# Kernel optimization log

Measured on AMD Instinct MI355X. Metric: run time of the kernel, lower is better.

## Reference

```python
import jax, jax.numpy as jnp
import numpy as np

SIGMA = 0.1
B, C, H, W = 2, 3, 64, 64


def setup_inputs() -> dict:
    key = jax.random.key(0)
    x = jax.random.uniform(key, (B, C, H, W), dtype=jnp.float32)
    return {"x": x}


def reference(x) -> jnp.ndarray:
    """Range-only bilateral filter: out[p] = sum_q K(p,q) x[q] / sum_q K(p,q),
    K(p,q) = exp(-((x_q - x_p)/sigma)^2), all-pairs over the H*W pixels,
    independently per (batch, channel)."""
    b, c, h, w = x.shape
    n = h * w
    xf = x.reshape(b, c, n)                      # [B,C,N]
    # pairwise intensity differences -> Gaussian range kernel [B,C,N,N]
    diff = xf[:, :, :, None] - xf[:, :, None, :]
    K = jnp.exp(-jnp.square(diff / SIGMA))
    num = jnp.einsum('bcpq,bcq->bcp', K, xf)     # weighted sum over source pixels
    den = jnp.sum(K, axis=-1)                    # normalization
    return (num / den).reshape(b, c, h, w)
```

## Files before the change

kernel.cpp:

```cpp
#include <hip/hip_runtime.h>

#define NSLICE 6
#define NPIX   4096
#define M      20

#define C0         0.088622693f
#define TWO_C0     0.177245385f
#define AEXP_LOG2  0.035597112f
#define DEN0       362.99854f

__global__ __launch_bounds__(256) void moments_kernel(
        const float* __restrict__ x, float* __restrict__ ws) {
    const int mi = blockIdx.x;
    const int s  = blockIdx.y;
    const float fm = (float)(mi + 1);
    const int tid = threadIdx.x;
    const float4* x4 = (const float4*)(x + s * NPIX);

    float Sc = 0.f, Ss = 0.f, Tc = 0.f, Ts = 0.f, X = 0.f;
    #pragma unroll
    for (int j = 0; j < NPIX / 4 / 256; ++j) {
        float4 v4 = x4[j * 256 + tid];
        float vv[4] = {v4.x, v4.y, v4.z, v4.w};
        #pragma unroll
        for (int k = 0; k < 4; ++k) {
            float v   = vv[k];
            float arg = 0.5f * fm * v;
            float sn  = __builtin_amdgcn_sinf(arg);
            float cn  = __builtin_amdgcn_cosf(arg);
            Sc += cn;  Ss += sn;
            Tc = fmaf(v, cn, Tc);
            Ts = fmaf(v, sn, Ts);
            X += v;
        }
    }

    #pragma unroll
    for (int off = 1; off < 64; off <<= 1) {
        Sc += __shfl_xor(Sc, off);  Ss += __shfl_xor(Ss, off);
        Tc += __shfl_xor(Tc, off);  Ts += __shfl_xor(Ts, off);
        X  += __shfl_xor(X,  off);
    }
    __shared__ float red[4][5];
    const int w = tid >> 6;
    if ((tid & 63) == 0) {
        red[w][0] = Sc; red[w][1] = Ss; red[w][2] = Tc; red[w][3] = Ts; red[w][4] = X;
    }
    __syncthreads();
    if (tid == 0) {
        float sc = 0.f, ss = 0.f, tc = 0.f, ts = 0.f, xx = 0.f;
        #pragma unroll
        for (int ww = 0; ww < 4; ++ww) {
            sc += red[ww][0]; ss += red[ww][1]; tc += red[ww][2];
            ts += red[ww][3]; xx += red[ww][4];
        }
        float coef = TWO_C0 * __builtin_amdgcn_exp2f(-AEXP_LOG2 * fm * fm);
        float* f = ws + (s * (M + 1) + (mi + 1)) * 4;
        f[0] = coef * sc;  f[1] = coef * ss;
        f[2] = coef * tc;  f[3] = coef * ts;
        if (mi == 0) {
            float* f0 = ws + s * (M + 1) * 4;
            f0[0] = DEN0;  f0[1] = C0 * xx;  f0[2] = 0.f;  f0[3] = 0.f;
        }
    }
}

__global__ __launch_bounds__(512) void recombine_kernel(
        const float* __restrict__ x, const float* __restrict__ ws,
        float* __restrict__ out) {
    const int s = blockIdx.y;
    const int p = blockIdx.x * 512 + threadIdx.x;
    __shared__ __align__(16) float fin[(M + 1) * 4];
    if (threadIdx.x < (M + 1) * 4)
        fin[threadIdx.x] = ws[s * (M + 1) * 4 + threadIdx.x];
    __syncthreads();

    const float v  = x[s * NPIX + p];
    const float s1 = __builtin_amdgcn_sinf(0.5f * v);
    const float c1 = __builtin_amdgcn_cosf(0.5f * v);
    const float4* F = (const float4*)fin;

    float4 f0 = F[0], f1 = F[1];
    float den = f0.x, num = f0.y;
    den = fmaf(c1, f1.x, den);  den = fmaf(s1, f1.y, den);
    num = fmaf(c1, f1.z, num);  num = fmaf(s1, f1.w, num);

    const float tc = c1 + c1;
    float cm2 = 1.f, sm2 = 0.f, cm1 = c1, sm1 = s1;
    #pragma unroll
    for (int m = 2; m <= M; ++m) {
        float cn = fmaf(tc, cm1, -cm2);
        float sn = fmaf(tc, sm1, -sm2);
        cm2 = cm1; cm1 = cn; sm2 = sm1; sm1 = sn;
        float4 f = F[m];
        den = fmaf(cn, f.x, den);  den = fmaf(sn, f.y, den);
        num = fmaf(cn, f.z, num);  num = fmaf(sn, f.w, num);
    }
    out[s * NPIX + p] = num / den;
}

extern "C" void kernel_launch(void* const* d_in, const int* in_sizes, int n_in,
                              void* d_out, int out_size, void* d_ws, size_t ws_size,
                              hipStream_t stream) {
    const float* x = (const float*)d_in[0];
    float* out = (float*)d_out;
    float* ws  = (float*)d_ws;
    moments_kernel<<<dim3(M, NSLICE), dim3(256), 0, stream>>>(x, ws);
    recombine_kernel<<<dim3(NPIX / 512, NSLICE), dim3(512), 0, stream>>>(x, ws, out);
}
```

Before: 54.59 us.

## Fuse moments and recombine kernels into one launch with redundant per-block moments

Merges the two kernels into a single launch with 48 blocks. Each block recomputes all 20 Fourier moments for its slice before evaluating its 512 output pixels, so no workspace round-trip and no second launch are needed. Within the moment pass each thread covers 5 harmonics using a Chebyshev recurrence seeded from a few sin/cos calls, instead of one harmonic per block. The cost is that every block redoes the full moment reduction over 4096 pixels, which is eight times redundant work per slice.

```diff
diff --git a/kernel.cpp b/kernel.cpp
--- a/kernel.cpp
+++ b/kernel.cpp
@@ -3,90 +3,110 @@
 #define NSLICE 6
 #define NPIX   4096
 #define M      20
+#define TPB    512
 
 #define C0         0.088622693f
 #define TWO_C0     0.177245385f
 #define AEXP_LOG2  0.035597112f
 #define DEN0       362.99854f
 
-__global__ __launch_bounds__(256) void moments_kernel(
-        const float* __restrict__ x, float* __restrict__ ws) {
-    const int mi = blockIdx.x;
-    const int s  = blockIdx.y;
-    const float fm = (float)(mi + 1);
+__global__ __launch_bounds__(TPB) void bilateral_fused(
+        const float* __restrict__ x, float* __restrict__ out) {
+    __shared__ float4 part4[32][4][5];
+    __shared__ float  xpart[32];
+    __shared__ __align__(16) float fin[(M + 1) * 4];
+
     const int tid = threadIdx.x;
-    const float4* x4 = (const float4*)(x + s * NPIX);
+    const int s   = blockIdx.x >> 3;
+    const int bt  = blockIdx.x & 7;
+    const float* xs = x + s * NPIX;
 
-    float Sc = 0.f, Ss = 0.f, Tc = 0.f, Ts = 0.f, X = 0.f;
+    const int fg  = tid & 3;
+    const int set = tid >> 2;
+    const float a = (float)(5 * fg);
+
+    float Sc[5], Ss[5], Tc[5], Ts[5], X = 0.f;
     #pragma unroll
-    for (int j = 0; j < NPIX / 4 / 256; ++j) {
-        float4 v4 = x4[j * 256 + tid];
+    for (int k = 0; k < 5; ++k) { Sc[k]=0.f; Ss[k]=0.f; Tc[k]=0.f; Ts[k]=0.f; }
+
+    const float4* x4 = (const float4*)xs;
+    #pragma unroll
+    for (int j = 0; j < 8; ++j) {
+        float4 v4 = x4[set * 8 + j];
         float vv[4] = {v4.x, v4.y, v4.z, v4.w};
         #pragma unroll
-        for (int k = 0; k < 4; ++k) {
-            float v   = vv[k];
-            float arg = 0.5f * fm * v;
-            float sn  = __builtin_amdgcn_sinf(arg);
-            float cn  = __builtin_amdgcn_cosf(arg);
-            Sc += cn;  Ss += sn;
-            Tc = fmaf(v, cn, Tc);
-            Ts = fmaf(v, sn, Ts);
+        for (int u = 0; u < 4; ++u) {
+            float v = vv[u];
             X += v;
+            float h  = 0.5f * v;
+            float c1 = __builtin_amdgcn_cosf(h);
+            float tc = c1 + c1;
+            float cp = __builtin_amdgcn_cosf(a * h);
+            float sp = __builtin_amdgcn_sinf(a * h);
+            float cc = __builtin_amdgcn_cosf(fmaf(a, h, h));
+            float ss = __builtin_amdgcn_sinf(fmaf(a, h, h));
+            #pragma unroll
+            for (int k = 0; k < 5; ++k) {
+                Sc[k] += cc;  Ss[k] += ss;
+                Tc[k] = fmaf(v, cc, Tc[k]);  Ts[k] = fmaf(v, ss, Ts[k]);
+                float cn = fmaf(tc, cc, -cp);
+                float sn = fmaf(tc, ss, -sp);
+                cp = cc; cc = cn; sp = ss; ss = sn;
+            }
         }
     }
 
     #pragma unroll
-    for (int off = 1; off < 64; off <<= 1) {
-        Sc += __shfl_xor(Sc, off);  Ss += __shfl_xor(Ss, off);
-        Tc += __shfl_xor(Tc, off);  Ts += __shfl_xor(Ts, off);
-        X  += __shfl_xor(X,  off);
+    for (int off = 4; off <= 8; off <<= 1) {
+        X += __shfl_xor(X, off);
+        #pragma unroll
+        for (int k = 0; k < 5; ++k) {
+            Sc[k] += __shfl_xor(Sc[k], off);
+            Ss[k] += __shfl_xor(Ss[k], off);
+            Tc[k] += __shfl_xor(Tc[k], off);
+            Ts[k] += __shfl_xor(Ts[k], off);
+        }
     }
-    __shared__ float red[4][5];
-    const int w = tid >> 6;
-    if ((tid & 63) == 0) {
-        red[w][0] = Sc; red[w][1] = Ss; red[w][2] = Tc; red[w][3] = Ts; red[w][4] = X;
+    const int lane = tid & 63;
+    const int wv   = tid >> 6;
+    if ((lane & 12) == 0) {
+        int g = (wv << 2) | (lane >> 4);
+        #pragma unroll
+        for (int k = 0; k < 5; ++k)
+            part4[g][fg][k] = make_float4(Sc[k], Ss[k], Tc[k], Ts[k]);
+        if ((lane & 15) == 0) xpart[g] = X;
     }
     __syncthreads();
-    if (tid == 0) {
-        float sc = 0.f, ss = 0.f, tc = 0.f, ts = 0.f, xx = 0.f;
-        #pragma unroll
-        for (int ww = 0; ww < 4; ++ww) {
-            sc += red[ww][0]; ss += red[ww][1]; tc += red[ww][2];
-            ts += red[ww][3]; xx += red[ww][4];
-        }
-        float coef = TWO_C0 * __builtin_amdgcn_exp2f(-AEXP_LOG2 * fm * fm);
-        float* f = ws + (s * (M + 1) + (mi + 1)) * 4;
-        f[0] = coef * sc;  f[1] = coef * ss;
-        f[2] = coef * tc;  f[3] = coef * ts;
-        if (mi == 0) {
-            float* f0 = ws + s * (M + 1) * 4;
-            f0[0] = DEN0;  f0[1] = C0 * xx;  f0[2] = 0.f;  f0[3] = 0.f;
+
+    if (tid < 81) {
+        if (tid == 80) {
+            float xx = 0.f;
+            #pragma unroll
+            for (int g = 0; g < 32; ++g) xx += xpart[g];
+            fin[0] = DEN0;  fin[1] = C0 * xx;  fin[2] = 0.f;  fin[3] = 0.f;
+        } else {
+            const float* pf = (const float*)part4;
+            float sum = 0.f;
+            #pragma unroll
+            for (int g = 0; g < 32; ++g) sum += pf[g * 80 + tid];
+            int m = (tid >> 2) + 1;
+            float fm = (float)m;
+            float coef = TWO_C0 * __builtin_amdgcn_exp2f(-AEXP_LOG2 * fm * fm);
+            fin[m * 4 + (tid & 3)] = coef * sum;
         }
     }
-}
-
-__global__ __launch_bounds__(512) void recombine_kernel(
-        const float* __restrict__ x, const float* __restrict__ ws,
-        float* __restrict__ out) {
-    const int s = blockIdx.y;
-    const int p = blockIdx.x * 512 + threadIdx.x;
-    __shared__ __align__(16) float fin[(M + 1) * 4];
-    if (threadIdx.x < (M + 1) * 4)
-        fin[threadIdx.x] = ws[s * (M + 1) * 4 + threadIdx.x];
     __syncthreads();
 
-    const float v  = x[s * NPIX + p];
-    const float s1 = __builtin_amdgcn_sinf(0.5f * v);
-    const float c1 = __builtin_amdgcn_cosf(0.5f * v);
+    const int p = bt * TPB + tid;
+    float v  = xs[p];
+    float h  = 0.5f * v;
+    float s1 = __builtin_amdgcn_sinf(h);
+    float c1 = __builtin_amdgcn_cosf(h);
     const float4* F = (const float4*)fin;
-
     float4 f0 = F[0], f1 = F[1];
-    float den = f0.x, num = f0.y;
-    den = fmaf(c1, f1.x, den);  den = fmaf(s1, f1.y, den);
-    num = fmaf(c1, f1.z, num);  num = fmaf(s1, f1.w, num);
-
-    const float tc = c1 + c1;
-    float cm2 = 1.f, sm2 = 0.f, cm1 = c1, sm1 = s1;
+    float den = fmaf(c1, f1.x, f0.x);  den = fmaf(s1, f1.y, den);
+    float num = fmaf(c1, f1.z, f0.y);  num = fmaf(s1, f1.w, num);
+    float tc = c1 + c1, cm2 = 1.f, sm2 = 0.f, cm1 = c1, sm1 = s1;
     #pragma unroll
     for (int m = 2; m <= M; ++m) {
         float cn = fmaf(tc, cm1, -cm2);
@@ -104,7 +124,5 @@
                               hipStream_t stream) {
     const float* x = (const float*)d_in[0];
     float* out = (float*)d_out;
-    float* ws  = (float*)d_ws;
-    moments_kernel<<<dim3(M, NSLICE), dim3(256), 0, stream>>>(x, ws);
-    recombine_kernel<<<dim3(NPIX / 512, NSLICE), dim3(512), 0, stream>>>(x, ws, out);
+    bilateral_fused<<<dim3(NSLICE * 8), dim3(TPB), 0, stream>>>(x, out);
 }
```

Measured after the change: 56.86 us. 1.04x slower.
